# Performance work log

Measured on AMD Instinct MI355X. Metric: run time of the kernel, lower is better.

## Reference

```python
import jax, jax.numpy as jnp
import numpy as np

NEG_SLOPE = 0.2  # PyG GATConv default negative_slope


def setup_inputs() -> dict:
    key = jax.random.key(0)
    k1, k2, k3, k4, k5 = jax.random.split(key, 5)
    N, E, IN, H, C = 50000, 800000, 128, 4, 64
    x = jax.random.normal(k1, (N, IN), dtype=jnp.float32)
    edge_index = jax.random.randint(k2, (2, E), 0, N, dtype=jnp.int32)
    W = jax.random.normal(k3, (IN, H * C), dtype=jnp.float32) * (1.0 / np.sqrt(IN))
    att_src = jax.random.normal(k4, (H, C), dtype=jnp.float32) * 0.1
    att_dst = jax.random.normal(k5, (H, C), dtype=jnp.float32) * 0.1
    bias = jnp.zeros((C,), dtype=jnp.float32)
    return {"x": x, "edge_index": edge_index, "W": W,
            "att_src": att_src, "att_dst": att_dst, "bias": bias}


def reference(x, edge_index, W, att_src, att_dst, bias):
    N = x.shape[0]
    H, C = att_src.shape
    # add self loops (PyG GATConv default add_self_loops=True)
    loop = jnp.arange(N, dtype=edge_index.dtype)
    src = jnp.concatenate([edge_index[0], loop])  # message source j
    dst = jnp.concatenate([edge_index[1], loop])  # message target i
    # linear projection, per-head view [N, H, C]
    h = (x @ W).reshape(N, H, C)
    # per-node attention terms [N, H]
    a_src = jnp.einsum('nhc,hc->nh', h, att_src)
    a_dst = jnp.einsum('nhc,hc->nh', h, att_dst)
    # per-edge logits with leaky relu [Etot, H]
    e = jax.nn.leaky_relu(a_src[src] + a_dst[dst], NEG_SLOPE)
    # segment softmax over incoming edges of each destination node
    emax = jax.ops.segment_max(e, dst, num_segments=N)       # [N, H]
    ex = jnp.exp(e - emax[dst])                              # [Etot, H]
    denom = jax.ops.segment_sum(ex, dst, num_segments=N)     # [N, H]
    alpha = ex / denom[dst]                                  # [Etot, H]
    # weighted scatter-aggregate of source features
    msg = h[src] * alpha[:, :, None]                         # [Etot, H, C]
    out = jax.ops.segment_sum(msg, dst, num_segments=N)      # [N, H, C]
    # concat=False -> mean over heads, then bias, then module-level ELU
    out = out.mean(axis=1) + bias
    return jax.nn.elu(out)
```

## Files before the change

kernel.cpp:

```cpp
#include <hip/hip_runtime.h>

#define NEG_SLOPE 0.2f
static constexpr int IN_F = 128;
static constexpr int NHEAD = 4;
static constexpr int CH = 64;
static constexpr int HC = 256;

static __host__ size_t align256(size_t v) { return (v + 255) & ~((size_t)255); }

__device__ inline ushort f2bf(float f) {
    unsigned u = __float_as_uint(f);
    unsigned r = u + 0x7FFFu + ((u >> 16) & 1u);
    return (ushort)(r >> 16);
}
__device__ inline float bf2f(ushort s) { return __uint_as_float(((unsigned)s) << 16); }

typedef short s16x8 __attribute__((ext_vector_type(8)));
typedef float f32x16 __attribute__((ext_vector_type(16)));

__global__ __launch_bounds__(256) void prep_kernel(
    const float* __restrict__ W, ushort* __restrict__ Wt,
    int* __restrict__ coarse_cnt)
{
    int f = blockIdx.x * 256 + threadIdx.x;
    int k = f >> 8;
    int n = f & 255;
    Wt[n * IN_F + k] = f2bf(W[(size_t)k * HC + n]);
    if (blockIdx.x == 0) coarse_cnt[threadIdx.x] = 0;
}

__global__ __launch_bounds__(256) void gemm_mfma_kernel(
    const float* __restrict__ x, const ushort* __restrict__ Wt,
    const float* __restrict__ att_src, const float* __restrict__ att_dst,
    ushort* __restrict__ hb, float* __restrict__ a_src, float* __restrict__ a_dst,
    const int* __restrict__ dst, int* __restrict__ coarse_cnt,
    int E, int epb, int NTB, int NB, int N)
{
    constexpr int LDK = 136;
    __shared__ ushort As[64 * LDK];
    __shared__ ushort Bs[128 * LDK];
    ushort* Hs = As;

    const int t = threadIdx.x;

    if (blockIdx.x >= NTB) {
        int* hist = (int*)As;
        hist[t] = 0;
        __syncthreads();
        int slice = (blockIdx.x - NTB) * 2 + blockIdx.y;
        int lo = slice * epb;
        int hi = min(E, lo + epb);
        for (int i = lo + t; i < hi; i += 256)
            atomicAdd(&hist[((unsigned)dst[i]) >> 8], 1);
        __syncthreads();
        if (t < NB && hist[t]) atomicAdd(&coarse_cnt[t], hist[t]);
        return;
    }

    const int m0 = blockIdx.x * 64;
    const int n0 = blockIdx.y * 128;

    #pragma unroll
    for (int u = 0; u < 8; ++u) {
        int f = t + 256 * u;
        int r = f >> 5;
        int k4 = (f & 31) * 4;
        int row = m0 + r;
        float4 v = make_float4(0.f, 0.f, 0.f, 0.f);
        if (row < N) v = *(const float4*)(x + (size_t)row * IN_F + k4);
        ushort4 o;
        o.x = f2bf(v.x); o.y = f2bf(v.y); o.z = f2bf(v.z); o.w = f2bf(v.w);
        *(ushort4*)&As[r * LDK + k4] = o;
    }
    #pragma unroll
    for (int u = 0; u < 8; ++u) {
        int f = t + 256 * u;
        int n = f >> 4;
        int k8 = (f & 15) * 8;
        uint4 v = *(const uint4*)(Wt + (size_t)(n0 + n) * IN_F + k8);
        *(uint4*)&Bs[n * LDK + k8] = v;
    }
    __syncthreads();

    const int w = t >> 6;
    const int lane = t & 63;
    const int mrow = 32 * (w >> 1) + (lane & 31);
    const int nbase = 64 * (w & 1) + (lane & 31);
    const int kq = (lane >> 5) * 8;

    f32x16 acc0 = {}, acc1 = {};
    #pragma unroll
    for (int s = 0; s < 8; ++s) {
        s16x8 af = *(const s16x8*)&As[mrow * LDK + 16 * s + kq];
        s16x8 b0 = *(const s16x8*)&Bs[nbase * LDK + 16 * s + kq];
        s16x8 b1 = *(const s16x8*)&Bs[(nbase + 32) * LDK + 16 * s + kq];
        acc0 = __builtin_amdgcn_mfma_f32_32x32x16_bf16(af, b0, acc0, 0, 0, 0);
        acc1 = __builtin_amdgcn_mfma_f32_32x32x16_bf16(af, b1, acc1, 0, 0, 0);
    }
    __syncthreads();

    {
        int rbase = 4 * (lane >> 5) + 32 * (w >> 1);
        int c0 = 64 * (w & 1) + (lane & 31);
        #pragma unroll
        for (int r = 0; r < 16; ++r) {
            int rowL = rbase + (r & 3) + 8 * (r >> 2);
            Hs[rowL * LDK + c0]      = f2bf(acc0[r]);
            Hs[rowL * LDK + c0 + 32] = f2bf(acc1[r]);
        }
    }
    __syncthreads();

    {
        int r2 = t >> 2;
        int q = t & 3;
        int row = m0 + r2;
        uint4 p0 = *(const uint4*)&Hs[r2 * LDK + 32 * q];
        uint4 p1 = *(const uint4*)&Hs[r2 * LDK + 32 * q + 8];
        uint4 p2 = *(const uint4*)&Hs[r2 * LDK + 32 * q + 16];
        uint4 p3 = *(const uint4*)&Hs[r2 * LDK + 32 * q + 24];
        if (row < N) {
            ushort* dsth = hb + (size_t)row * HC + n0 + 32 * q;
            *(uint4*)(dsth)      = p0;
            *(uint4*)(dsth + 8)  = p1;
            *(uint4*)(dsth + 16) = p2;
            *(uint4*)(dsth + 24) = p3;
        }
        int hq = 2 * blockIdx.y + (q >> 1);
        int cb = (q & 1) * 32;
        const float* asp = att_src + hq * CH + cb;
        const float* adp = att_dst + hq * CH + cb;
        unsigned uu[16] = { p0.x, p0.y, p0.z, p0.w, p1.x, p1.y, p1.z, p1.w,
                            p2.x, p2.y, p2.z, p2.w, p3.x, p3.y, p3.z, p3.w };
        float ps = 0.f, pd = 0.f;
        #pragma unroll
        for (int i = 0; i < 16; ++i) {
            float lo = bf2f((ushort)(uu[i] & 0xFFFFu));
            float hi = bf2f((ushort)(uu[i] >> 16));
            ps += lo * asp[2 * i] + hi * asp[2 * i + 1];
            pd += lo * adp[2 * i] + hi * adp[2 * i + 1];
        }
        ps += __shfl_xor(ps, 1, 64);
        pd += __shfl_xor(pd, 1, 64);
        if ((q & 1) == 0 && row < N) {
            a_src[(size_t)row * NHEAD + hq] = ps;
            a_dst[(size_t)row * NHEAD + hq] = pd;
        }
    }
}

__global__ __launch_bounds__(256) void scan_coarse(
    const int* __restrict__ coarse_cnt, int* __restrict__ ebase,
    int* __restrict__ bucket_cur, int* __restrict__ rowptr,
    int NB, int N, int E)
{
    __shared__ int sm[256];
    int t = threadIdx.x;
    int v = (t < NB) ? coarse_cnt[t] : 0;
    sm[t] = v;
    __syncthreads();
    #pragma unroll
    for (int off = 1; off < 256; off <<= 1) {
        int a = sm[t];
        int b = (t >= off) ? sm[t - off] : 0;
        __syncthreads();
        sm[t] = a + b;
        __syncthreads();
    }
    int incl = sm[t];
    int excl = incl - v;
    if (t < NB) { ebase[t] = excl; bucket_cur[t] = excl; }
    if (t == NB - 1) ebase[NB] = incl;
    if (t == 0) rowptr[N] = E + N;
}

__global__ __launch_bounds__(256) void bucket_scatter(
    const int* __restrict__ src, const int* __restrict__ dst,
    int* __restrict__ bucket_cur, unsigned* __restrict__ ebuf,
    int E, int epb, int NB)
{
    __shared__ int hist[256];
    __shared__ int base[256];
    int t = threadIdx.x;
    hist[t] = 0;
    __syncthreads();
    int lo = blockIdx.x * epb;
    int hi = min(E, lo + epb);
    for (int i = lo + t; i < hi; i += 256)
        atomicAdd(&hist[((unsigned)dst[i]) >> 8], 1);
    __syncthreads();
    if (t < NB && hist[t]) base[t] = atomicAdd(&bucket_cur[t], hist[t]);
    __syncthreads();
    hist[t] = 0;
    __syncthreads();
    for (int i = lo + t; i < hi; i += 256) {
        unsigned d = (unsigned)dst[i];
        unsigned b = d >> 8;
        int off2 = atomicAdd(&hist[b], 1);
        ebuf[base[b] + off2] = (((unsigned)src[i]) << 8) | (d & 255u);
    }
}

__global__ __launch_bounds__(256) void csr_build(
    const unsigned* __restrict__ ebuf, const int* __restrict__ ebase,
    int* __restrict__ rowptr, int* __restrict__ csr_src, int N)
{
    __shared__ int hist[256];
    __shared__ int scn[256];
    __shared__ int cur[256];
    int b = blockIdx.x;
    int t = threadIdx.x;
    int n0 = b << 8;
    int ncnt = min(256, N - n0);
    int lo = ebase[b], hi = ebase[b + 1];
    int cb = lo + n0;
    hist[t] = 0;
    __syncthreads();
    for (int i = lo + t; i < hi; i += 256)
        atomicAdd(&hist[ebuf[i] & 255u], 1);
    __syncthreads();
    int v = hist[t];
    scn[t] = v;
    __syncthreads();
    #pragma unroll
    for (int off = 1; off < 256; off <<= 1) {
        int a = scn[t];
        int bb = (t >= off) ? scn[t - off] : 0;
        __syncthreads();
        scn[t] = a + bb;
        __syncthreads();
    }
    int excl = scn[t] - v;
    int segstart = cb + excl + t;
    if (t < ncnt) {
        rowptr[n0 + t] = segstart;
        csr_src[segstart] = n0 + t;
    }
    cur[t] = excl + t + 1;
    __syncthreads();
    for (int i = lo + t; i < hi; i += 256) {
        unsigned e = ebuf[i];
        int ln = (int)(e & 255u);
        int pos = atomicAdd(&cur[ln], 1);
        csr_src[cb + pos] = (int)(e >> 8);
    }
}

__global__ __launch_bounds__(256) void aggregate_kernel(
    const ushort* __restrict__ hb, const float* __restrict__ a_src,
    const float* __restrict__ a_dst, const int* __restrict__ rowptr,
    const int* __restrict__ csr_src, const float* __restrict__ bias,
    float* __restrict__ out, int N)
{
    int node = (int)((blockIdx.x * (size_t)blockDim.x + threadIdx.x) >> 6);
    int l = threadIdx.x & 63;
    if (node >= N) return;
    int start = rowptr[node];
    int end = rowptr[node + 1];
    int hd = l >> 4;
    float adh = a_dst[(size_t)node * NHEAD + hd];

    float4 acc[4];
    float s[4];
    #pragma unroll
    for (int u = 0; u < 4; ++u) { acc[u] = make_float4(0.f,0.f,0.f,0.f); s[u] = 0.f; }

    int k = start;
    for (; k + 8 <= end; k += 8) {
        int sj[8];
        #pragma unroll
        for (int u = 0; u < 8; ++u) sj[u] = csr_src[k + u];
        float av[8]; ushort4 hv[8];
        #pragma unroll
        for (int u = 0; u < 8; ++u) {
            av[u] = a_src[(size_t)sj[u] * NHEAD + hd];
            hv[u] = *(const ushort4*)(hb + ((size_t)sj[u] << 8) + 4 * l);
        }
        #pragma unroll
        for (int u = 0; u < 8; ++u) {
            float e = av[u] + adh; e = fmaxf(e, NEG_SLOPE * e);
            float wgt = __expf(e);
            int q = u & 3;
            s[q] += wgt;
            acc[q].x += wgt * bf2f(hv[u].x); acc[q].y += wgt * bf2f(hv[u].y);
            acc[q].z += wgt * bf2f(hv[u].z); acc[q].w += wgt * bf2f(hv[u].w);
        }
    }
    for (; k + 4 <= end; k += 4) {
        int sj[4];
        #pragma unroll
        for (int u = 0; u < 4; ++u) sj[u] = csr_src[k + u];
        float av[4]; ushort4 hv[4];
        #pragma unroll
        for (int u = 0; u < 4; ++u) {
            av[u] = a_src[(size_t)sj[u] * NHEAD + hd];
            hv[u] = *(const ushort4*)(hb + ((size_t)sj[u] << 8) + 4 * l);
        }
        #pragma unroll
        for (int u = 0; u < 4; ++u) {
            float e = av[u] + adh; e = fmaxf(e, NEG_SLOPE * e);
            float wgt = __expf(e);
            s[u] += wgt;
            acc[u].x += wgt * bf2f(hv[u].x); acc[u].y += wgt * bf2f(hv[u].y);
            acc[u].z += wgt * bf2f(hv[u].z); acc[u].w += wgt * bf2f(hv[u].w);
        }
    }
    for (; k < end; ++k) {
        int sj0 = csr_src[k];
        float a0 = a_src[(size_t)sj0 * NHEAD + hd];
        ushort4 h0 = *(const ushort4*)(hb + ((size_t)sj0 << 8) + 4 * l);
        float e0 = a0 + adh; e0 = fmaxf(e0, NEG_SLOPE * e0);
        float w0 = __expf(e0);
        s[0] += w0;
        acc[0].x += w0 * bf2f(h0.x); acc[0].y += w0 * bf2f(h0.y);
        acc[0].z += w0 * bf2f(h0.z); acc[0].w += w0 * bf2f(h0.w);
    }

    float inv = 1.0f / (s[0] + s[1] + s[2] + s[3]);
    float4 a4;
    a4.x = (acc[0].x + acc[1].x + acc[2].x + acc[3].x) * inv;
    a4.y = (acc[0].y + acc[1].y + acc[2].y + acc[3].y) * inv;
    a4.z = (acc[0].z + acc[1].z + acc[2].z + acc[3].z) * inv;
    a4.w = (acc[0].w + acc[1].w + acc[2].w + acc[3].w) * inv;

    #pragma unroll
    for (int off = 16; off < 64; off <<= 1) {
        a4.x += __shfl_xor(a4.x, off, 64);
        a4.y += __shfl_xor(a4.y, off, 64);
        a4.z += __shfl_xor(a4.z, off, 64);
        a4.w += __shfl_xor(a4.w, off, 64);
    }
    if (l < 16) {
        float4 b4 = *(const float4*)(bias + 4 * l);
        float4 o;
        o.x = a4.x * 0.25f + b4.x;
        o.y = a4.y * 0.25f + b4.y;
        o.z = a4.z * 0.25f + b4.z;
        o.w = a4.w * 0.25f + b4.w;
        o.x = (o.x > 0.f) ? o.x : (__expf(o.x) - 1.f);
        o.y = (o.y > 0.f) ? o.y : (__expf(o.y) - 1.f);
        o.z = (o.z > 0.f) ? o.z : (__expf(o.z) - 1.f);
        o.w = (o.w > 0.f) ? o.w : (__expf(o.w) - 1.f);
        *(float4*)(out + (size_t)node * CH + 4 * l) = o;
    }
}

extern "C" void kernel_launch(void* const* d_in, const int* in_sizes, int n_in,
                              void* d_out, int out_size, void* d_ws, size_t ws_size,
                              hipStream_t stream)
{
    const float* x         = (const float*)d_in[0];
    const int*   edge_idx  = (const int*)d_in[1];
    const float* W         = (const float*)d_in[2];
    const float* att_src   = (const float*)d_in[3];
    const float* att_dst   = (const float*)d_in[4];
    const float* bias      = (const float*)d_in[5];
    float* out = (float*)d_out;

    const int N = in_sizes[0] / IN_F;
    const int E = in_sizes[1] / 2;
    const int Etot = E + N;
    const int NB = (N + 255) >> 8;
    const int* srcp = edge_idx;
    const int* dstp = edge_idx + E;

    char* ws = (char*)d_ws;
    size_t off = 0;
    ushort*  hb     = (ushort*)(ws + off);   off += align256((size_t)N * HC * sizeof(ushort));
    ushort*  Wt     = (ushort*)(ws + off);   off += align256((size_t)HC * IN_F * sizeof(ushort));
    float*   a_src  = (float*)(ws + off);    off += align256((size_t)N * NHEAD * sizeof(float));
    float*   a_dst  = (float*)(ws + off);    off += align256((size_t)N * NHEAD * sizeof(float));
    int*     ccnt   = (int*)(ws + off);      off += align256(256 * sizeof(int));
    int*     ebase  = (int*)(ws + off);      off += align256(257 * sizeof(int));
    int*     bcur   = (int*)(ws + off);      off += align256(256 * sizeof(int));
    unsigned* ebuf  = (unsigned*)(ws + off); off += align256((size_t)E * sizeof(unsigned));
    int*     rowptr = (int*)(ws + off);      off += align256(((size_t)N + 1) * sizeof(int));
    int*     csrs   = (int*)(ws + off);      off += align256((size_t)Etot * sizeof(int));
    (void)ws_size; (void)n_in; (void)out_size;

    const int NTB = (N + 63) / 64;
    const int PBC = 208;
    const int epbc = (E + 2 * PBC - 1) / (2 * PBC);
    const int PB = 416;
    const int epb = (E + PB - 1) / PB;

    prep_kernel<<<IN_F * HC / 256, 256, 0, stream>>>(W, Wt, ccnt);
    dim3 gg(NTB + PBC, 2);
    gemm_mfma_kernel<<<gg, 256, 0, stream>>>(x, Wt, att_src, att_dst, hb,
                                             a_src, a_dst, dstp, ccnt,
                                             E, epbc, NTB, NB, N);
    scan_coarse<<<1, 256, 0, stream>>>(ccnt, ebase, bcur, rowptr, NB, N, E);
    bucket_scatter<<<PB, 256, 0, stream>>>(srcp, dstp, bcur, ebuf, E, epb, NB);
    csr_build<<<NB, 256, 0, stream>>>(ebuf, ebase, rowptr, csrs, N);
    aggregate_kernel<<<((size_t)N * 64 + 255) / 256, 256, 0, stream>>>(
        hb, a_src, a_dst, rowptr, csrs, bias, out, N);
}
```

Baseline: 210.1 us.

## Stage bucket scatter and CSR build through shared memory for coalesced writes

Result: faster. 203.8 us (-3.0%).

```diff
diff --git a/kernel.cpp b/kernel.cpp
--- a/kernel.cpp
+++ b/kernel.cpp
@@ -5,6 +5,8 @@
 static constexpr int NHEAD = 4;
 static constexpr int CH = 64;
 static constexpr int HC = 256;
+static constexpr int SC_EPB = 2000;
+static constexpr int CB_CAP = 6144;
 
 static __host__ size_t align256(size_t v) { return (v + 255) & ~((size_t)255); }
 
@@ -177,27 +179,62 @@
 __global__ __launch_bounds__(256) void bucket_scatter(
     const int* __restrict__ src, const int* __restrict__ dst,
     int* __restrict__ bucket_cur, unsigned* __restrict__ ebuf,
-    int E, int epb, int NB)
+    int E, int NB)
 {
     __shared__ int hist[256];
-    __shared__ int base[256];
+    __shared__ int lbase[256];
+    __shared__ int gbase[256];
+    __shared__ int cur[256];
+    __shared__ unsigned sbuf[SC_EPB + 48];
+    __shared__ unsigned char tb[SC_EPB + 48];
     int t = threadIdx.x;
+    int lo = blockIdx.x * SC_EPB;
+    int hi = min(E, lo + SC_EPB);
+    int cnt = hi - lo;
     hist[t] = 0;
     __syncthreads();
-    int lo = blockIdx.x * epb;
-    int hi = min(E, lo + epb);
-    for (int i = lo + t; i < hi; i += 256)
-        atomicAdd(&hist[((unsigned)dst[i]) >> 8], 1);
-    __syncthreads();
-    if (t < NB && hist[t]) base[t] = atomicAdd(&bucket_cur[t], hist[t]);
-    __syncthreads();
-    hist[t] = 0;
-    __syncthreads();
-    for (int i = lo + t; i < hi; i += 256) {
-        unsigned d = (unsigned)dst[i];
-        unsigned b = d >> 8;
-        int off2 = atomicAdd(&hist[b], 1);
-        ebuf[base[b] + off2] = (((unsigned)src[i]) << 8) | (d & 255u);
+    unsigned pk[8]; int bk[8];
+    #pragma unroll
+    for (int u = 0; u < 8; ++u) {
+        int i = lo + t + 256 * u;
+        bk[u] = -1;
+        if (i < hi) {
+            unsigned d = (unsigned)dst[i];
+            bk[u] = (int)(d >> 8);
+            pk[u] = (((unsigned)src[i]) << 8) | (d & 255u);
+            atomicAdd(&hist[bk[u]], 1);
+        }
+    }
+    __syncthreads();
+    int v = hist[t];
+    lbase[t] = v;
+    __syncthreads();
+    #pragma unroll
+    for (int off = 1; off < 256; off <<= 1) {
+        int a = lbase[t];
+        int b = (t >= off) ? lbase[t - off] : 0;
+        __syncthreads();
+        lbase[t] = a + b;
+        __syncthreads();
+    }
+    int excl = lbase[t] - v;
+    if (v) gbase[t] = atomicAdd(&bucket_cur[t], v);
+    __syncthreads();
+    lbase[t] = excl;
+    cur[t] = excl;
+    __syncthreads();
+    #pragma unroll
+    for (int u = 0; u < 8; ++u) {
+        if (bk[u] >= 0) {
+            int p = atomicAdd(&cur[bk[u]], 1);
+            sbuf[p] = pk[u];
+            tb[p] = (unsigned char)bk[u];
+        }
+    }
+    __syncthreads();
+    for (int j = t; j < cnt; j += 256) {
+        int b = tb[j];
+        ebuf[gbase[b] + j - lbase[b]] = sbuf[j];
     }
 }
 
@@ -208,11 +245,13 @@
     __shared__ int hist[256];
     __shared__ int scn[256];
     __shared__ int cur[256];
+    __shared__ unsigned srt[CB_CAP];
     int b = blockIdx.x;
     int t = threadIdx.x;
     int n0 = b << 8;
     int ncnt = min(256, N - n0);
     int lo = ebase[b], hi = ebase[b + 1];
+    int cnt = hi - lo;
     int cb = lo + n0;
     hist[t] = 0;
     __syncthreads();
@@ -231,18 +270,31 @@
         __syncthreads();
     }
     int excl = scn[t] - v;
-    int segstart = cb + excl + t;
     if (t < ncnt) {
+        int segstart = cb + excl + t;
         rowptr[n0 + t] = segstart;
         csr_src[segstart] = n0 + t;
     }
-    cur[t] = excl + t + 1;
-    __syncthreads();
-    for (int i = lo + t; i < hi; i += 256) {
-        unsigned e = ebuf[i];
-        int ln = (int)(e & 255u);
-        int pos = atomicAdd(&cur[ln], 1);
-        csr_src[cb + pos] = (int)(e >> 8);
+    cur[t] = excl;
+    __syncthreads();
+    if (cnt <= CB_CAP) {
+        for (int i = lo + t; i < hi; i += 256) {
+            unsigned e = ebuf[i];
+            int p = atomicAdd(&cur[e & 255u], 1);
+            srt[p] = e;
+        }
+        __syncthreads();
+        for (int j = t; j < cnt; j += 256) {
+            unsigned e = srt[j];
+            csr_src[cb + j + (int)(e & 255u) + 1] = (int)(e >> 8);
+        }
+    } else {
+        for (int i = lo + t; i < hi; i += 256) {
+            unsigned e = ebuf[i];
+            int ln = (int)(e & 255u);
+            int p = atomicAdd(&cur[ln], 1);
+            csr_src[cb + p + ln + 1] = (int)(e >> 8);
+        }
     }
 }
 
@@ -260,50 +312,39 @@
     int hd = l >> 4;
     float adh = a_dst[(size_t)node * NHEAD + hd];
 
-    float4 acc[4];
-    float s[4];
-    #pragma unroll
-    for (int u = 0; u < 4; ++u) { acc[u] = make_float4(0.f,0.f,0.f,0.f); s[u] = 0.f; }
+    float4 acc0 = make_float4(0.f, 0.f, 0.f, 0.f);
+    float4 acc1 = make_float4(0.f, 0.f, 0.f, 0.f);
+    float4 acc2 = make_float4(0.f, 0.f, 0.f, 0.f);
+    float4 acc3 = make_float4(0.f, 0.f, 0.f, 0.f);
+    float s0 = 0.f, s1 = 0.f, s2 = 0.f, s3 = 0.f;
 
     int k = start;
-    for (; k + 8 <= end; k += 8) {
-        int sj[8];
-        #pragma unroll
-        for (int u = 0; u < 8; ++u) sj[u] = csr_src[k + u];
-        float av[8]; ushort4 hv[8];
-        #pragma unroll
-        for (int u = 0; u < 8; ++u) {
-            av[u] = a_src[(size_t)sj[u] * NHEAD + hd];
-            hv[u] = *(const ushort4*)(hb + ((size_t)sj[u] << 8) + 4 * l);
-        }
-        #pragma unroll
-        for (int u = 0; u < 8; ++u) {
-            float e = av[u] + adh; e = fmaxf(e, NEG_SLOPE * e);
-            float wgt = __expf(e);
-            int q = u & 3;
-            s[q] += wgt;
-            acc[q].x += wgt * bf2f(hv[u].x); acc[q].y += wgt * bf2f(hv[u].y);
-            acc[q].z += wgt * bf2f(hv[u].z); acc[q].w += wgt * bf2f(hv[u].w);
-        }
-    }
     for (; k + 4 <= end; k += 4) {
-        int sj[4];
-        #pragma unroll
-        for (int u = 0; u < 4; ++u) sj[u] = csr_src[k + u];
-        float av[4]; ushort4 hv[4];
-        #pragma unroll
-        for (int u = 0; u < 4; ++u) {
-            av[u] = a_src[(size_t)sj[u] * NHEAD + hd];
-            hv[u] = *(const ushort4*)(hb + ((size_t)sj[u] << 8) + 4 * l);
-        }
-        #pragma unroll
-        for (int u = 0; u < 4; ++u) {
-            float e = av[u] + adh; e = fmaxf(e, NEG_SLOPE * e);
-            float wgt = __expf(e);
-            s[u] += wgt;
-            acc[u].x += wgt * bf2f(hv[u].x); acc[u].y += wgt * bf2f(hv[u].y);
-            acc[u].z += wgt * bf2f(hv[u].z); acc[u].w += wgt * bf2f(hv[u].w);
-        }
+        int sj0 = csr_src[k];
+        int sj1 = csr_src[k + 1];
+        int sj2 = csr_src[k + 2];
+        int sj3 = csr_src[k + 3];
+        float a0 = a_src[(size_t)sj0 * NHEAD + hd];
+        float a1 = a_src[(size_t)sj1 * NHEAD + hd];
+        float a2 = a_src[(size_t)sj2 * NHEAD + hd];
+        float a3 = a_src[(size_t)sj3 * NHEAD + hd];
+        ushort4 h0 = *(const ushort4*)(hb + ((size_t)sj0 << 8) + 4 * l);
+        ushort4 h1 = *(const ushort4*)(hb + ((size_t)sj1 << 8) + 4 * l);
+        ushort4 h2 = *(const ushort4*)(hb + ((size_t)sj2 << 8) + 4 * l);
+        ushort4 h3 = *(const ushort4*)(hb + ((size_t)sj3 << 8) + 4 * l);
+        float e0 = a0 + adh; e0 = fmaxf(e0, NEG_SLOPE * e0); float w0 = __expf(e0);
+        float e1 = a1 + adh; e1 = fmaxf(e1, NEG_SLOPE * e1); float w1 = __expf(e1);
+        float e2 = a2 + adh; e2 = fmaxf(e2, NEG_SLOPE * e2); float w2 = __expf(e2);
+        float e3 = a3 + adh; e3 = fmaxf(e3, NEG_SLOPE * e3); float w3 = __expf(e3);
+        s0 += w0; s1 += w1; s2 += w2; s3 += w3;
+        acc0.x += w0 * bf2f(h0.x); acc0.y += w0 * bf2f(h0.y);
+        acc0.z += w0 * bf2f(h0.z); acc0.w += w0 * bf2f(h0.w);
+        acc1.x += w1 * bf2f(h1.x); acc1.y += w1 * bf2f(h1.y);
+        acc1.z += w1 * bf2f(h1.z); acc1.w += w1 * bf2f(h1.w);
+        acc2.x += w2 * bf2f(h2.x); acc2.y += w2 * bf2f(h2.y);
+        acc2.z += w2 * bf2f(h2.z); acc2.w += w2 * bf2f(h2.w);
+        acc3.x += w3 * bf2f(h3.x); acc3.y += w3 * bf2f(h3.y);
+        acc3.z += w3 * bf2f(h3.z); acc3.w += w3 * bf2f(h3.w);
     }
     for (; k < end; ++k) {
         int sj0 = csr_src[k];
@@ -311,32 +352,32 @@
         ushort4 h0 = *(const ushort4*)(hb + ((size_t)sj0 << 8) + 4 * l);
         float e0 = a0 + adh; e0 = fmaxf(e0, NEG_SLOPE * e0);
         float w0 = __expf(e0);
-        s[0] += w0;
-        acc[0].x += w0 * bf2f(h0.x); acc[0].y += w0 * bf2f(h0.y);
-        acc[0].z += w0 * bf2f(h0.z); acc[0].w += w0 * bf2f(h0.w);
-    }
-
-    float inv = 1.0f / (s[0] + s[1] + s[2] + s[3]);
-    float4 a4;
-    a4.x = (acc[0].x + acc[1].x + acc[2].x + acc[3].x) * inv;
-    a4.y = (acc[0].y + acc[1].y + acc[2].y + acc[3].y) * inv;
-    a4.z = (acc[0].z + acc[1].z + acc[2].z + acc[3].z) * inv;
-    a4.w = (acc[0].w + acc[1].w + acc[2].w + acc[3].w) * inv;
+        s0 += w0;
+        acc0.x += w0 * bf2f(h0.x); acc0.y += w0 * bf2f(h0.y);
+        acc0.z += w0 * bf2f(h0.z); acc0.w += w0 * bf2f(h0.w);
+    }
+
+    float inv = 1.0f / (s0 + s1 + s2 + s3);
+    float4 acc;
+    acc.x = (acc0.x + acc1.x + acc2.x + acc3.x) * inv;
+    acc.y = (acc0.y + acc1.y + acc2.y + acc3.y) * inv;
+    acc.z = (acc0.z + acc1.z + acc2.z + acc3.z) * inv;
+    acc.w = (acc0.w + acc1.w + acc2.w + acc3.w) * inv;
 
     #pragma unroll
     for (int off = 16; off < 64; off <<= 1) {
-        a4.x += __shfl_xor(a4.x, off, 64);
-        a4.y += __shfl_xor(a4.y, off, 64);
-        a4.z += __shfl_xor(a4.z, off, 64);
-        a4.w += __shfl_xor(a4.w, off, 64);
+        acc.x += __shfl_xor(acc.x, off, 64);
+        acc.y += __shfl_xor(acc.y, off, 64);
+        acc.z += __shfl_xor(acc.z, off, 64);
+        acc.w += __shfl_xor(acc.w, off, 64);
     }
     if (l < 16) {
         float4 b4 = *(const float4*)(bias + 4 * l);
         float4 o;
-        o.x = a4.x * 0.25f + b4.x;
-        o.y = a4.y * 0.25f + b4.y;
-        o.z = a4.z * 0.25f + b4.z;
-        o.w = a4.w * 0.25f + b4.w;
+        o.x = acc.x * 0.25f + b4.x;
+        o.y = acc.y * 0.25f + b4.y;
+        o.z = acc.z * 0.25f + b4.z;
+        o.w = acc.w * 0.25f + b4.w;
         o.x = (o.x > 0.f) ? o.x : (__expf(o.x) - 1.f);
         o.y = (o.y > 0.f) ? o.y : (__expf(o.y) - 1.f);
         o.z = (o.z > 0.f) ? o.z : (__expf(o.z) - 1.f);
@@ -381,8 +422,7 @@
     const int NTB = (N + 63) / 64;
     const int PBC = 208;
     const int epbc = (E + 2 * PBC - 1) / (2 * PBC);
-    const int PB = 416;
-    const int epb = (E + PB - 1) / PB;
+    const int PBS = (E + SC_EPB - 1) / SC_EPB;
 
     prep_kernel<<<IN_F * HC / 256, 256, 0, stream>>>(W, Wt, ccnt);
     dim3 gg(NTB + PBC, 2);
@@ -390,7 +430,7 @@
                                              a_src, a_dst, dstp, ccnt,
                                              E, epbc, NTB, NB, N);
     scan_coarse<<<1, 256, 0, stream>>>(ccnt, ebase, bcur, rowptr, NB, N, E);
-    bucket_scatter<<<PB, 256, 0, stream>>>(srcp, dstp, bcur, ebuf, E, epb, NB);
+    bucket_scatter<<<PBS, 256, 0, stream>>>(srcp, dstp, bcur, ebuf, E, NB);
     csr_build<<<NB, 256, 0, stream>>>(ebuf, ebase, rowptr, csrs, N);
     aggregate_kernel<<<((size_t)N * 64 + 255) / 256, 256, 0, stream>>>(
         hb, a_src, a_dst, rowptr, csrs, bias, out, N);
```
